# Performance work log

Hardware: AMD Instinct MI355X
Metric: run time of the kernel (lower is better)

The kernel has to match this reference:

```python
import jax, jax.numpy as jnp
import numpy as np

D_MODEL = 1024
N_HEADS = 16
D_FF = 4 * D_MODEL
CTX = 2048
EPS = 1e-5


def setup_inputs() -> dict:
    key = jax.random.key(0)
    ks = jax.random.split(key, 8)
    s = 0.02
    z = jax.random.normal(ks[0], (2, CTX, D_MODEL), dtype=jnp.float32)
    W_Q = jax.random.normal(ks[1], (D_MODEL, D_MODEL), dtype=jnp.float32) * s
    W_K = jax.random.normal(ks[2], (D_MODEL, D_MODEL), dtype=jnp.float32) * s
    W_V = jax.random.normal(ks[3], (D_MODEL, D_MODEL), dtype=jnp.float32) * s
    W_O = jax.random.normal(ks[4], (D_MODEL, D_MODEL), dtype=jnp.float32) * s
    W_fc = jax.random.normal(ks[5], (D_MODEL, D_FF), dtype=jnp.float32) * s
    W_proj = jax.random.normal(ks[6], (D_FF, D_MODEL), dtype=jnp.float32) * s
    g1 = jnp.ones((D_MODEL,), dtype=jnp.float32)
    g2 = jnp.ones((D_MODEL,), dtype=jnp.float32)
    return {"z": z, "W_Q": W_Q, "W_K": W_K, "W_V": W_V, "W_O": W_O,
            "W_fc": W_fc, "W_proj": W_proj, "g1": g1, "g2": g2}


def rmsnorm(x, gain):
    rms = jnp.sqrt(jnp.sum(x * x, axis=-1, keepdims=True) / x.shape[-1] + EPS)
    return (x / rms) * gain


def gelu_erf(x):
    return x * 0.5 * (1.0 + jax.lax.erf(x / jnp.sqrt(2.0).astype(x.dtype)))


def attention(zn, W_Q, W_K, W_V, W_O):
    B, T, D = zn.shape
    H = N_HEADS
    dh = D // H
    # [B,T,D] -> [B,H,T,dh]
    def split(x):
        return x.reshape(B, T, H, dh).transpose(0, 2, 1, 3)
    Q = split(zn @ W_Q)
    K = split(zn @ W_K)
    V = split(zn @ W_V)
    scores = jnp.einsum('bhtd,bhsd->bhts', Q, K) / jnp.sqrt(jnp.float32(dh))
    causal = jnp.triu(jnp.ones((T, T), dtype=bool), k=1)  # True above diagonal -> masked
    scores = jnp.where(causal[None, None], -jnp.inf, scores)
    weights = jax.nn.softmax(scores, axis=-1)
    ctx = jnp.einsum('bhts,bhsd->bhtd', weights, V)
    ctx = ctx.transpose(0, 2, 1, 3).reshape(B, T, D)
    return ctx @ W_O


def reference(z, W_Q, W_K, W_V, W_O, W_fc, W_proj, g1, g2):
    # pre-norm GPT block: z + attn(norm1(z)); then + ffn(norm2(z))
    z = z + attention(rmsnorm(z, g1), W_Q, W_K, W_V, W_O)
    h = rmsnorm(z, g2)
    ffn = gelu_erf(h @ W_fc) @ W_proj
    return z + ffn
```

## Files before the change

kernel.cpp:

```cpp
#include <hip/hip_runtime.h>
#include <hip/hip_bf16.h>
#include <math.h>


typedef __bf16 bf16x8 __attribute__((ext_vector_type(8)));
typedef float  f32x4  __attribute__((ext_vector_type(4)));

#define MFMA_16x16x32_BF16(A, B, C) __builtin_amdgcn_mfma_f32_16x16x32_bf16((A), (B), (C), 0, 0, 0)

#define GLDS16(g, l) __builtin_amdgcn_global_load_lds( \
    (const __attribute__((address_space(1))) void*)(g), \
    (__attribute__((address_space(3))) void*)(l), 16, 0, 0)

__global__ __launch_bounds__(256) void fused_head_kernel(
    const float* __restrict__ W_Q, const float* __restrict__ W_K,
    const float* __restrict__ W_V, const float* __restrict__ W_O,
    const float* __restrict__ W_fc, const float* __restrict__ W_proj,
    __bf16* __restrict__ WtQKV, __bf16* __restrict__ WtO,
    __bf16* __restrict__ Wtfc, __bf16* __restrict__ Wtproj,
    const float* __restrict__ z, const float* __restrict__ g1,
    __bf16* __restrict__ zn)
{
    const int id = blockIdx.x;
    if (id >= 12288) {
        const int row = id - 12288, t = threadIdx.x;
        const float4 v = ((const float4*)(z + (size_t)row * 1024))[t];
        float ss = v.x * v.x + v.y * v.y + v.z * v.z + v.w * v.w;
#pragma unroll
        for (int m = 1; m < 64; m <<= 1) ss += __shfl_xor(ss, m);
        __shared__ float red[4];
        const int wid = t >> 6, lane = t & 63;
        if (lane == 0) red[wid] = ss;
        __syncthreads();
        const float tot = red[0] + red[1] + red[2] + red[3];
        const float inv = rsqrtf(tot * (1.0f / 1024.0f) + 1e-5f);
        const float4 gv = ((const float4*)g1)[t];
        __bf16* o = zn + (size_t)row * 1024 + t * 4;
        o[0] = (__bf16)(v.x * inv * gv.x);
        o[1] = (__bf16)(v.y * inv * gv.y);
        o[2] = (__bf16)(v.z * inv * gv.z);
        o[3] = (__bf16)(v.w * inv * gv.w);
        return;
    }
    const float* src;
    __bf16* dst;
    int K, N, nx, t;
    if (id < 4096) {
        const int wsel = id >> 10;
        t = id & 1023;
        src = (wsel == 0) ? W_Q : (wsel == 1) ? W_K : (wsel == 2) ? W_V : W_O;
        dst = (wsel < 3) ? (WtQKV + (size_t)wsel * 1048576) : WtO;
        K = 1024; N = 1024; nx = 32;
    } else if (id < 8192) {
        t = id - 4096; src = W_fc; dst = Wtfc; K = 1024; N = 4096; nx = 128;
    } else {
        t = id - 8192; src = W_proj; dst = Wtproj; K = 4096; N = 1024; nx = 32;
    }
    const int n0 = (t % nx) * 32, k0 = (t / nx) * 32;

    __shared__ float tile[32][33];
    const int c = threadIdx.x & 31, r = threadIdx.x >> 5;
#pragma unroll
    for (int i = 0; i < 4; ++i)
        tile[r + 8 * i][c] = src[(size_t)(k0 + r + 8 * i) * N + n0 + c];
    __syncthreads();
#pragma unroll
    for (int i = 0; i < 4; ++i)
        dst[(size_t)(n0 + r + 8 * i) * K + k0 + c] = (__bf16)tile[c][r + 8 * i];
}

__global__ __launch_bounds__(256) void rmsnorm_kernel(
    const float* __restrict__ x, const float* __restrict__ gain,
    __bf16* __restrict__ out)
{
    const int row = blockIdx.x, t = threadIdx.x;
    const float4 v = ((const float4*)(x + (size_t)row * 1024))[t];
    float ss = v.x * v.x + v.y * v.y + v.z * v.z + v.w * v.w;
#pragma unroll
    for (int m = 1; m < 64; m <<= 1) ss += __shfl_xor(ss, m);
    __shared__ float red[4];
    const int wid = t >> 6, lane = t & 63;
    if (lane == 0) red[wid] = ss;
    __syncthreads();
    const float tot = red[0] + red[1] + red[2] + red[3];
    const float inv = rsqrtf(tot * (1.0f / 1024.0f) + 1e-5f);
    const float4 gv = ((const float4*)gain)[t];
    __bf16* o = out + (size_t)row * 1024 + t * 4;
    o[0] = (__bf16)(v.x * inv * gv.x);
    o[1] = (__bf16)(v.y * inv * gv.y);
    o[2] = (__bf16)(v.z * inv * gv.z);
    o[3] = (__bf16)(v.w * inv * gv.w);
}

__global__ __launch_bounds__(256) void reduce_add_kernel(
    float* __restrict__ out, const float* __restrict__ p0,
    const float* __restrict__ p1, int n4)
{
    for (int i = blockIdx.x * 256 + threadIdx.x; i < n4; i += gridDim.x * 256) {
        const float4 a = ((const float4*)p0)[i];
        const float4 b = ((const float4*)p1)[i];
        float4 o = ((float4*)out)[i];
        o.x += a.x + b.x; o.y += a.y + b.y;
        o.z += a.z + b.z; o.w += a.w + b.w;
        ((float4*)out)[i] = o;
    }
}

template <int EPI>
__device__ __forceinline__ void epi_write(
    void* outp, const float* res, int N, int rowg, int colg, float v)
{
    if constexpr (EPI == 1) {
        const size_t idx = (size_t)rowg * N + colg;
        ((float*)outp)[idx] = res[idx] + v;
    } else if constexpr (EPI == 2) {
        const size_t idx = (size_t)rowg * N + colg;
        const float u = v * (1.0f + 0.044715f * v * v) * 2.3022585093f;
        const float r = __builtin_amdgcn_rcpf(1.0f + exp2f(u));
        ((__bf16*)outp)[idx] = (__bf16)(v - v * r);
    } else if constexpr (EPI == 3) {
        const size_t idx = (size_t)rowg * N + colg;
        ((float*)outp)[idx] += v;
    } else {
        __bf16* base = (__bf16*)outp;
        const int seg = colg >> 10;
        const int cg = colg & 1023;
        if (seg < 2) {
            base[(size_t)seg * 4194304 + (size_t)rowg * 1024 + cg] = (__bf16)v;
        } else {
            const int tt = rowg & 2047;
            const int r32 = tt & 31;
            const int p = ((r32 & 12) << 1) | ((r32 >> 2) & 4) | (r32 & 3);
            base[8388608 +
                 ((size_t)((rowg >> 11) * 16 + (cg >> 6)) * 64 + (cg & 63)) * 2048 +
                 ((tt & ~31) | p)] = (__bf16)v;
        }
    }
}

template <int EPI>
__global__ __launch_bounds__(512, 2) void gemm256(
    const __bf16* __restrict__ A, const __bf16* __restrict__ Bt,
    void* __restrict__ outp, const float* __restrict__ res,
    int M, int N, int K)
{
    __shared__ __bf16 As[2][2][128 * 64];
    __shared__ __bf16 Bs[2][2][128 * 64];
    const int tid = threadIdx.x;

    const int gx = gridDim.x, nwg = gx * gridDim.y;
    int bid = blockIdx.y * gx + blockIdx.x;
    if ((nwg & 7) == 0) bid = (bid & 7) * (nwg >> 3) + (bid >> 3);
    const int m0 = (bid / gx) * 256, n0 = (bid % gx) * 256;

    const int lane = tid & 63, w = tid >> 6;
    const int wr = w >> 2, wc = w & 3;
    const int lr = lane & 15, g = lane >> 4;
    const int srow8 = lane >> 3, schunk = (lane & 7) ^ srow8;
    const int xk = lr & 7;
    const int wch = wc >> 1, bro = (wc & 1) * 64;

    const __bf16* Ab = A + (size_t)m0 * K;
    const __bf16* Bb = Bt + (size_t)n0 * K;

    auto STG = [&](const __bf16* gb, __bf16* lds, int kt, int half) {
        const __bf16* src = gb + (size_t)(half * 128) * K + (kt << 6);
#pragma unroll
        for (int j = 0; j < 2; ++j) {
            const int sidx = j * 8 + w;
            GLDS16(src + (size_t)(sidx * 8 + srow8) * K + schunk * 8, lds + sidx * 512);
        }
    };

    f32x4 acc[8][4] = {};
    bf16x8 af[2][4], bf[2][4];

#define LAF(BUF, QM) do {                                                       \
    _Pragma("unroll") for (int i_ = 0; i_ < 4; ++i_)                            \
    _Pragma("unroll") for (int kk_ = 0; kk_ < 2; ++kk_)                         \
        af[kk_][i_] = *(const bf16x8*)&As[BUF][wr]                              \
            [((QM) * 64 + i_ * 16 + lr) * 64 + (((kk_ * 4 + g) ^ xk) << 3)];    \
    } while (0)

#define LBF(BUF, QN) do {                                                       \
    _Pragma("unroll") for (int i_ = 0; i_ < 2; ++i_)                            \
    _Pragma("unroll") for (int kk_ = 0; kk_ < 2; ++kk_)                         \
        bf[kk_][(QN) * 2 + i_] = *(const bf16x8*)&Bs[BUF][wch]                  \
            [(bro + ((QN) * 2 + i_) * 16 + lr) * 64 + (((kk_ * 4 + g) ^ xk) << 3)]; \
    } while (0)

#define MMQ(QM, QN) do {                                                        \
    __builtin_amdgcn_s_setprio(1);                                              \
    _Pragma("unroll") for (int kk_ = 0; kk_ < 2; ++kk_)                         \
    _Pragma("unroll") for (int i_ = 0; i_ < 4; ++i_)                            \
    _Pragma("unroll") for (int n_ = 0; n_ < 2; ++n_)                            \
        acc[(QM) * 4 + i_][(QN) * 2 + n_] = MFMA_16x16x32_BF16(                 \
            af[kk_][i_], bf[kk_][(QN) * 2 + n_], acc[(QM) * 4 + i_][(QN) * 2 + n_]); \
    __builtin_amdgcn_s_setprio(0);                                              \
    } while (0)

#define BAR()  __builtin_amdgcn_s_barrier()
#define VMC(N_) asm volatile("s_waitcnt vmcnt(" #N_ ")" ::: "memory")
#define SGB0() __builtin_amdgcn_sched_barrier(0)

    const int nt = K >> 6, niter = nt >> 1;

    STG(Ab, &As[0][0][0], 0, 0); STG(Ab, &As[0][1][0], 0, 1);
    STG(Bb, &Bs[0][0][0], 0, 0); STG(Bb, &Bs[0][1][0], 0, 1);
    STG(Bb, &Bs[1][0][0], 1, 0); STG(Bb, &Bs[1][1][0], 1, 1);

    for (int i = 0; i < niter - 1; ++i) {
        const int t1 = 2 * i + 1;
        STG(Ab, &As[1][0][0], t1, 0);
        VMC(6); BAR(); SGB0();
        LAF(0, 0); LBF(0, 0); MMQ(0, 0); BAR();
        LBF(0, 1); STG(Ab, &As[1][1][0], t1, 1); BAR(); MMQ(0, 1); BAR();
        LAF(0, 1); STG(Bb, &Bs[0][0][0], t1 + 1, 0); BAR(); MMQ(1, 0); BAR();
        STG(Bb, &Bs[0][1][0], t1 + 1, 1); BAR(); MMQ(1, 1); BAR();
        STG(Ab, &As[0][0][0], t1 + 1, 0);
        VMC(6); BAR(); SGB0();
        LAF(1, 0); LBF(1, 0); MMQ(0, 0); BAR();
        LBF(1, 1); STG(Ab, &As[0][1][0], t1 + 1, 1); BAR(); MMQ(0, 1); BAR();
        LAF(1, 1); STG(Bb, &Bs[1][0][0], t1 + 2, 0); BAR(); MMQ(1, 0); BAR();
        STG(Bb, &Bs[1][1][0], t1 + 2, 1); BAR(); MMQ(1, 1); BAR();
    }
    {
        STG(Ab, &As[1][0][0], nt - 1, 0);
        VMC(6); BAR(); SGB0();
        LAF(0, 0); LBF(0, 0); MMQ(0, 0); BAR();
        LBF(0, 1); STG(Ab, &As[1][1][0], nt - 1, 1); BAR(); MMQ(0, 1); BAR();
        LAF(0, 1); BAR(); MMQ(1, 0); BAR();
        BAR(); MMQ(1, 1); BAR();
        VMC(0); BAR(); SGB0();
        LAF(1, 0); LBF(1, 0); MMQ(0, 0); BAR();
        LBF(1, 1); BAR(); MMQ(0, 1); BAR();
        LAF(1, 1); BAR(); MMQ(1, 0); BAR();
        BAR(); MMQ(1, 1); BAR();
    }
#undef LAF
#undef LBF
#undef MMQ
#undef BAR
#undef VMC
#undef SGB0

#pragma unroll
    for (int mi = 0; mi < 8; ++mi)
#pragma unroll
        for (int ni = 0; ni < 4; ++ni) {
            const int colg = n0 + wc * 64 + ni * 16 + lr;
#pragma unroll
            for (int r = 0; r < 4; ++r) {
                const int rowg = m0 + wr * 128 + mi * 16 + 4 * g + r;
                epi_write<EPI>(outp, res, N, rowg, colg, acc[mi][ni][r]);
            }
        }
}

template <int BM, int BN, int EPI>
__global__ __launch_bounds__(256) void gemm_bf16(
    const __bf16* __restrict__ A, const __bf16* __restrict__ Bt,
    void* __restrict__ outp, const float* __restrict__ res,
    int M, int N, int K, int Kld)
{
    __shared__ __bf16 As[2][BM * 64];
    __shared__ __bf16 Bs[2][BN * 64];
    const int tid = threadIdx.x;

    const int gx = gridDim.x, nwg = gx * gridDim.y;
    int bid = blockIdx.y * gx + blockIdx.x;
    if ((nwg & 7) == 0) bid = (bid & 7) * (nwg >> 3) + (bid >> 3);
    const int m0 = (bid / gx) * BM, n0 = (bid % gx) * BN;

    const int lane = tid & 63, w = tid >> 6;
    const int wm = w >> 1, wn = w & 1;
    const int lr = lane & 15, g = lane >> 4;
    const int srow = lane >> 3;
    const int scol = ((lane & 7) ^ srow) * 8;
    const int xr8 = lr & 7;

    constexpr int MI = BM / 32, NI = BN / 32;
    f32x4 acc[MI][NI] = {};

    const __bf16* Abase = A + (size_t)m0 * Kld + blockIdx.z * K;
    const __bf16* Bbase = Bt + (size_t)n0 * Kld + blockIdx.z * K;

    auto STAGE = [&](int kb, int buf) {
#pragma unroll
        for (int j = 0; j < BM / 32; ++j) {
            const int s = j * 4 + w;
            GLDS16(Abase + (size_t)(s * 8 + srow) * Kld + kb + scol, &As[buf][s * 512]);
        }
#pragma unroll
        for (int j = 0; j < BN / 32; ++j) {
            const int s = j * 4 + w;
            GLDS16(Bbase + (size_t)(s * 8 + srow) * Kld + kb + scol, &Bs[buf][s * 512]);
        }
    };

    const int nt = K >> 6;
    STAGE(0, 0);
    __syncthreads();

    for (int t = 0; t < nt; ++t) {
        const int cur = t & 1;
        if (t + 1 < nt) STAGE((t + 1) << 6, cur ^ 1);

        bf16x8 af[2][MI], bfr[2][NI];
#pragma unroll
        for (int kk = 0; kk < 2; ++kk) {
#pragma unroll
            for (int i = 0; i < MI; ++i)
                af[kk][i] = *(const bf16x8*)
                    &As[cur][(wm * (BM / 2) + i * 16 + lr) * 64 + (((kk * 4 + g) ^ xr8) << 3)];
#pragma unroll
            for (int i = 0; i < NI; ++i)
                bfr[kk][i] = *(const bf16x8*)
                    &Bs[cur][(wn * (BN / 2) + i * 16 + lr) * 64 + (((kk * 4 + g) ^ xr8) << 3)];
        }
#pragma unroll
        for (int kk = 0; kk < 2; ++kk)
#pragma unroll
            for (int mi = 0; mi < MI; ++mi)
#pragma unroll
                for (int ni = 0; ni < NI; ++ni)
                    acc[mi][ni] = MFMA_16x16x32_BF16(af[kk][mi], bfr[kk][ni], acc[mi][ni]);
        if (t + 1 < nt) __syncthreads();
    }

#pragma unroll
    for (int mi = 0; mi < MI; ++mi)
#pragma unroll
        for (int ni = 0; ni < NI; ++ni) {
            const int colg = n0 + wn * (BN / 2) + ni * 16 + lr;
#pragma unroll
            for (int r = 0; r < 4; ++r) {
                const int rowg = m0 + wm * (BM / 2) + mi * 16 + 4 * g + r;
                const float v = acc[mi][ni][r];
                if constexpr (EPI == 5) {
                    float* pout = (blockIdx.z == 0) ? (float*)outp : (float*)(void*)res;
                    pout[(size_t)rowg * N + colg] = v;
                } else {
                    epi_write<EPI>(outp, res, N, rowg, colg, v);
                }
            }
        }
}

__global__ __launch_bounds__(512) void attn_kernel(
    const __bf16* __restrict__ Q, const __bf16* __restrict__ Kb,
    const __bf16* __restrict__ Vt, __bf16* __restrict__ ctx)
{
    const int Dm = 1024, T = 2048;
    const int tid = threadIdx.x;
    const int w = tid >> 6, lane = tid & 63;
    const int lr = lane & 15, g = lane >> 4;
    const int bx = blockIdx.x;
    const int j = bx >> 5, bh = bx & 31, b = bh >> 4, h = bh & 15;
    const int qc = (j < 8) ? j : 23 - j;
    const int qbase = qc * 128 + w * 16;
    const size_t rowoff = (size_t)b * T;
    const __bf16* Qp = Q + rowoff * Dm + h * 64;
    const __bf16* Kp = Kb + rowoff * Dm + h * 64;
    const __bf16* Vtp = Vt + (size_t)bh * 64 * 2048;

    __shared__ __bf16 Ks[2][64 * 64];
    __shared__ __bf16 Vs[2][64 * 64];

    bf16x8 qf0 = *(const bf16x8*)&Qp[(size_t)(qbase + lr) * Dm + g * 8];
    bf16x8 qf1 = *(const bf16x8*)&Qp[(size_t)(qbase + lr) * Dm + 32 + g * 8];
    const float qsc = 0.125f * 1.44269504088896340736f;
#pragma unroll
    for (int jj = 0; jj < 8; ++jj) {
        qf0[jj] = (__bf16)((float)qf0[jj] * qsc);
        qf1[jj] = (__bf16)((float)qf1[jj] * qsc);
    }

    const int srow = lane >> 3;
    const int schunk = (lane & 7) ^ srow;
    const int wrow = w * 8 + srow;

    f32x4 acc[4] = {};
    float m_s = -__builtin_inff(), l_s = 0.0f;
    const int nsteps = 2 * qc + 2;
    const f32x4 zacc = {0.0f, 0.0f, 0.0f, 0.0f};
    const int xr = (lr & 7) << 3;
    const int qg = qbase + lr;

    GLDS16(Kp + (size_t)wrow * Dm + schunk * 8, &Ks[0][(w * 8) * 64]);
    GLDS16(Vtp + (size_t)wrow * T + schunk * 8, &Vs[0][(w * 8) * 64]);
    __syncthreads();

    for (int t = 0; t < nsteps; ++t) {
        const int kvb = t * 64, cur = t & 1;
        if (t + 1 < nsteps) {
            GLDS16(Kp + (size_t)(kvb + 64 + wrow) * Dm + schunk * 8,
                   &Ks[cur ^ 1][(w * 8) * 64]);
            GLDS16(Vtp + (size_t)wrow * T + kvb + 64 + schunk * 8,
                   &Vs[cur ^ 1][(w * 8) * 64]);
        }

        if (kvb <= qbase + 15) {
            float sv[4][4];
#pragma unroll
            for (int s4 = 0; s4 < 4; ++s4) {
                const int kv0 = kvb + s4 * 16;
                if (kv0 <= qbase + 15) {
                    const int row = s4 * 16 + lr;
                    const bf16x8 kfa = *(const bf16x8*)&Ks[cur][row * 64 + ((g * 8) ^ xr)];
                    const bf16x8 kfb = *(const bf16x8*)&Ks[cur][row * 64 + ((32 + g * 8) ^ xr)];
                    f32x4 st = MFMA_16x16x32_BF16(kfa, qf0, zacc);
                    st = MFMA_16x16x32_BF16(kfb, qf1, st);
                    const bool domask = (kv0 + 15 > qbase);
#pragma unroll
                    for (int r = 0; r < 4; ++r) {
                        float x = st[r];
                        if (domask && (kv0 + 4 * g + r > qg)) x = -__builtin_inff();
                        sv[s4][r] = x;
                    }
                } else {
#pragma unroll
                    for (int r = 0; r < 4; ++r) sv[s4][r] = -__builtin_inff();
                }
            }

            float tm = sv[0][0];
#pragma unroll
            for (int s4 = 0; s4 < 4; ++s4)
#pragma unroll
                for (int r = 0; r < 4; ++r) tm = fmaxf(tm, sv[s4][r]);
            tm = fmaxf(tm, __shfl_xor(tm, 16));
            tm = fmaxf(tm, __shfl_xor(tm, 32));

            float m_use = m_s;
            if (!__all(tm - m_s <= 11.5f)) {
                m_use = fmaxf(m_s, tm);
                const float corr = exp2f(m_s - m_use);
                l_s *= corr;
                float cr[4];
#pragma unroll
                for (int r = 0; r < 4; ++r) cr[r] = __shfl(corr, 4 * g + r);
#pragma unroll
                for (int ct = 0; ct < 4; ++ct) {
                    acc[ct][0] *= cr[0]; acc[ct][1] *= cr[1];
                    acc[ct][2] *= cr[2]; acc[ct][3] *= cr[3];
                }
                m_s = m_use;
            }

            float rs = 0.0f;
#pragma unroll
            for (int s4 = 0; s4 < 4; ++s4)
#pragma unroll
                for (int r = 0; r < 4; ++r) {
                    sv[s4][r] = exp2f(sv[s4][r] - m_use);
                    rs += sv[s4][r];
                }
            rs += __shfl_xor(rs, 16);
            rs += __shfl_xor(rs, 32);
            l_s += rs;

            bf16x8 pa0, pa1;
#pragma unroll
            for (int r = 0; r < 4; ++r) {
                pa0[r] = (__bf16)sv[0][r];
                pa0[4 + r] = (__bf16)sv[1][r];
                pa1[r] = (__bf16)sv[2][r];
                pa1[4 + r] = (__bf16)sv[3][r];
            }
            const bool liveB = (kvb + 32 <= qbase + 15);
#pragma unroll
            for (int ct = 0; ct < 4; ++ct) {
                const __bf16* vrow = &Vs[cur][(ct * 16 + lr) * 64];
                const bf16x8 vf = *(const bf16x8*)&vrow[(8 * g) ^ xr];
                acc[ct] = MFMA_16x16x32_BF16(pa0, vf, acc[ct]);
                if (liveB) {
                    const bf16x8 vf2 = *(const bf16x8*)&vrow[(32 + 8 * g) ^ xr];
                    acc[ct] = MFMA_16x16x32_BF16(pa1, vf2, acc[ct]);
                }
            }
        }
        __syncthreads();
    }

    const float il = __builtin_amdgcn_rcpf(l_s);
    float dn[4];
#pragma unroll
    for (int r = 0; r < 4; ++r) dn[r] = __shfl(il, 4 * g + r);
#pragma unroll
    for (int ct = 0; ct < 4; ++ct)
#pragma unroll
        for (int r = 0; r < 4; ++r)
            ctx[(rowoff + qbase + 4 * g + r) * Dm + h * 64 + ct * 16 + lr] =
                (__bf16)(acc[ct][r] * dn[r]);
}

extern "C" void kernel_launch(void* const* d_in, const int* in_sizes, int n_in,
                              void* d_out, int out_size, void* d_ws, size_t ws_size,
                              hipStream_t stream)
{
    (void)in_sizes; (void)n_in; (void)out_size; (void)ws_size;
    const float* z      = (const float*)d_in[0];
    const float* W_Q    = (const float*)d_in[1];
    const float* W_K    = (const float*)d_in[2];
    const float* W_V    = (const float*)d_in[3];
    const float* W_O    = (const float*)d_in[4];
    const float* W_fc   = (const float*)d_in[5];
    const float* W_proj = (const float*)d_in[6];
    const float* g1     = (const float*)d_in[7];
    const float* g2     = (const float*)d_in[8];
    float* out = (float*)d_out;

    char* ws = (char*)d_ws;
    const size_t MB = (size_t)1 << 20;
    __bf16* WtQKV  = (__bf16*)(ws + 0 * MB);
    __bf16* WtO    = (__bf16*)(ws + 6 * MB);
    __bf16* Wtfc   = (__bf16*)(ws + 8 * MB);
    __bf16* Wtproj = (__bf16*)(ws + 16 * MB);
    __bf16* zn     = (__bf16*)(ws + 24 * MB);
    __bf16* Qb     = (__bf16*)(ws + 32 * MB);
    __bf16* Kbuf   = (__bf16*)(ws + 40 * MB);
    __bf16* Vtb    = (__bf16*)(ws + 48 * MB);
    __bf16* ffn1   = (__bf16*)(ws + 40 * MB);
    float*  part0  = (float*)(ws + 0 * MB);
    float*  part1  = (float*)(ws + 24 * MB);
    __bf16* ctx    = zn;
    __bf16* hb     = Qb;

    const int Tt = 2048, Dm = 1024, Bb = 2, M = Bb * Tt, DFF = 4096;
    const dim3 blk256(256), blk512(512);

    fused_head_kernel<<<16384, blk256, 0, stream>>>(
        W_Q, W_K, W_V, W_O, W_fc, W_proj, WtQKV, WtO, Wtfc, Wtproj, z, g1, zn);

    gemm_bf16<128, 128, 4><<<dim3(24, 32), blk256, 0, stream>>>(
        zn, WtQKV, Qb, nullptr, M, 3072, Dm, Dm);

    attn_kernel<<<512, blk512, 0, stream>>>(Qb, Kbuf, Vtb, ctx);

    gemm_bf16<128, 64, 1><<<dim3(16, 32), blk256, 0, stream>>>(
        ctx, WtO, out, z, M, Dm, Dm, Dm);

    rmsnorm_kernel<<<M, blk256, 0, stream>>>(out, g2, hb);

    gemm256<2><<<dim3(16, 16), blk512, 0, stream>>>(
        hb, Wtfc, ffn1, nullptr, M, DFF, Dm);

    gemm_bf16<128, 128, 5><<<dim3(8, 32, 2), blk256, 0, stream>>>(
        ffn1, Wtproj, part0, (const float*)part1, M, Dm, DFF / 2, DFF);

    reduce_add_kernel<<<2048, blk256, 0, stream>>>(out, part0, part1, M * Dm / 4);
}
```

Measured before the change: 250.4 us.

## Double the attention KV tile from 64 to 128 keys per step

The flash-attention loop now processes 128 keys per iteration instead of 64. This halves the number of barrier-synchronised steps and prefetch issues, with K/V staging split into two loads per thread and a new XOR swizzle for the wider V tile. In exchange it doubles shared memory per block, increases register pressure (sv now holds 8x4 scores), and wastes more masked work on the diagonal tiles.

```diff
diff --git a/kernel.cpp b/kernel.cpp
--- a/kernel.cpp
+++ b/kernel.cpp
@@ -364,8 +364,8 @@
     const __bf16* Kp = Kb + rowoff * Dm + h * 64;
     const __bf16* Vtp = Vt + (size_t)bh * 64 * 2048;
 
-    __shared__ __bf16 Ks[2][64 * 64];
-    __shared__ __bf16 Vs[2][64 * 64];
+    __shared__ __bf16 Ks[2][128 * 64];
+    __shared__ __bf16 Vs[2][64 * 128];
 
     bf16x8 qf0 = *(const bf16x8*)&Qp[(size_t)(qbase + lr) * Dm + g * 8];
     bf16x8 qf1 = *(const bf16x8*)&Qp[(size_t)(qbase + lr) * Dm + 32 + g * 8];
@@ -376,107 +376,113 @@
         qf1[jj] = (__bf16)((float)qf1[jj] * qsc);
     }
 
-    const int srow = lane >> 3;
-    const int schunk = (lane & 7) ^ srow;
-    const int wrow = w * 8 + srow;
+    const int ksrow = lane >> 3;
+    const int kschunk = (lane & 7) ^ ksrow;
+    const int vsrow = lane >> 4;
 
     f32x4 acc[4] = {};
     float m_s = -__builtin_inff(), l_s = 0.0f;
-    const int nsteps = 2 * qc + 2;
+    const int nsteps = qc + 1;
     const f32x4 zacc = {0.0f, 0.0f, 0.0f, 0.0f};
-    const int xr = (lr & 7) << 3;
+    const int x8 = lr & 7;
     const int qg = qbase + lr;
 
-    GLDS16(Kp + (size_t)wrow * Dm + schunk * 8, &Ks[0][(w * 8) * 64]);
-    GLDS16(Vtp + (size_t)wrow * T + schunk * 8, &Vs[0][(w * 8) * 64]);
+    auto STAGE = [&](int kvb, int buf) {
+#pragma unroll
+        for (int jj = 0; jj < 2; ++jj) {
+            const int krow = w * 16 + jj * 8;
+            GLDS16(Kp + (size_t)(kvb + krow + ksrow) * Dm + kschunk * 8,
+                   &Ks[buf][krow * 64]);
+            const int vrow = w * 8 + jj * 4;
+            const int vchunk = (lane & 15) ^ ((vrow + vsrow) & 15);
+            GLDS16(Vtp + (size_t)(vrow + vsrow) * T + kvb + vchunk * 8,
+                   &Vs[buf][vrow * 128]);
+        }
+    };
+
+    STAGE(0, 0);
     __syncthreads();
 
     for (int t = 0; t < nsteps; ++t) {
-        const int kvb = t * 64, cur = t & 1;
-        if (t + 1 < nsteps) {
-            GLDS16(Kp + (size_t)(kvb + 64 + wrow) * Dm + schunk * 8,
-                   &Ks[cur ^ 1][(w * 8) * 64]);
-            GLDS16(Vtp + (size_t)wrow * T + kvb + 64 + schunk * 8,
-                   &Vs[cur ^ 1][(w * 8) * 64]);
-        }
-
-        if (kvb <= qbase + 15) {
-            float sv[4][4];
-#pragma unroll
-            for (int s4 = 0; s4 < 4; ++s4) {
-                const int kv0 = kvb + s4 * 16;
-                if (kv0 <= qbase + 15) {
-                    const int row = s4 * 16 + lr;
-                    const bf16x8 kfa = *(const bf16x8*)&Ks[cur][row * 64 + ((g * 8) ^ xr)];
-                    const bf16x8 kfb = *(const bf16x8*)&Ks[cur][row * 64 + ((32 + g * 8) ^ xr)];
-                    f32x4 st = MFMA_16x16x32_BF16(kfa, qf0, zacc);
-                    st = MFMA_16x16x32_BF16(kfb, qf1, st);
-                    const bool domask = (kv0 + 15 > qbase);
-#pragma unroll
-                    for (int r = 0; r < 4; ++r) {
-                        float x = st[r];
-                        if (domask && (kv0 + 4 * g + r > qg)) x = -__builtin_inff();
-                        sv[s4][r] = x;
-                    }
-                } else {
-#pragma unroll
-                    for (int r = 0; r < 4; ++r) sv[s4][r] = -__builtin_inff();
+        const int kvb = t * 128, cur = t & 1;
+        if (t + 1 < nsteps) STAGE(kvb + 128, cur ^ 1);
+
+        float sv[8][4];
+#pragma unroll
+        for (int s4 = 0; s4 < 8; ++s4) {
+            const int kv0 = kvb + s4 * 16;
+            if (kv0 <= qbase + 15) {
+                const int row = s4 * 16 + lr;
+                const bf16x8 kfa = *(const bf16x8*)&Ks[cur][row * 64 + ((g ^ x8) << 3)];
+                const bf16x8 kfb = *(const bf16x8*)&Ks[cur][row * 64 + (((4 + g) ^ x8) << 3)];
+                f32x4 st = MFMA_16x16x32_BF16(kfa, qf0, zacc);
+                st = MFMA_16x16x32_BF16(kfb, qf1, st);
+                const bool domask = (kv0 + 15 > qbase);
+#pragma unroll
+                for (int r = 0; r < 4; ++r) {
+                    float x = st[r];
+                    if (domask && (kv0 + 4 * g + r > qg)) x = -__builtin_inff();
+                    sv[s4][r] = x;
                 }
-            }
-
-            float tm = sv[0][0];
-#pragma unroll
-            for (int s4 = 0; s4 < 4; ++s4)
-#pragma unroll
-                for (int r = 0; r < 4; ++r) tm = fmaxf(tm, sv[s4][r]);
-            tm = fmaxf(tm, __shfl_xor(tm, 16));
-            tm = fmaxf(tm, __shfl_xor(tm, 32));
-
-            float m_use = m_s;
-            if (!__all(tm - m_s <= 11.5f)) {
-                m_use = fmaxf(m_s, tm);
-                const float corr = exp2f(m_s - m_use);
-                l_s *= corr;
-                float cr[4];
-#pragma unroll
-                for (int r = 0; r < 4; ++r) cr[r] = __shfl(corr, 4 * g + r);
-#pragma unroll
-                for (int ct = 0; ct < 4; ++ct) {
-                    acc[ct][0] *= cr[0]; acc[ct][1] *= cr[1];
-                    acc[ct][2] *= cr[2]; acc[ct][3] *= cr[3];
-                }
-                m_s = m_use;
-            }
-
-            float rs = 0.0f;
-#pragma unroll
-            for (int s4 = 0; s4 < 4; ++s4)
-#pragma unroll
-                for (int r = 0; r < 4; ++r) {
-                    sv[s4][r] = exp2f(sv[s4][r] - m_use);
-                    rs += sv[s4][r];
-                }
-            rs += __shfl_xor(rs, 16);
-            rs += __shfl_xor(rs, 32);
-            l_s += rs;
-
-            bf16x8 pa0, pa1;
+            } else {
+#pragma unroll
+                for (int r = 0; r < 4; ++r) sv[s4][r] = -__builtin_inff();
+            }
+        }
+
+        float tm = sv[0][0];
+#pragma unroll
+        for (int s4 = 0; s4 < 8; ++s4)
+#pragma unroll
+            for (int r = 0; r < 4; ++r) tm = fmaxf(tm, sv[s4][r]);
+        tm = fmaxf(tm, __shfl_xor(tm, 16));
+        tm = fmaxf(tm, __shfl_xor(tm, 32));
+
+        float m_use = m_s;
+        if (!__all(tm - m_s <= 11.5f)) {
+            m_use = fmaxf(m_s, tm);
+            const float corr = exp2f(m_s - m_use);
+            l_s *= corr;
+            float cr[4];
+#pragma unroll
+            for (int r = 0; r < 4; ++r) cr[r] = __shfl(corr, 4 * g + r);
+#pragma unroll
+            for (int ct = 0; ct < 4; ++ct) {
+                acc[ct][0] *= cr[0]; acc[ct][1] *= cr[1];
+                acc[ct][2] *= cr[2]; acc[ct][3] *= cr[3];
+            }
+            m_s = m_use;
+        }
+
+        float rs = 0.0f;
+#pragma unroll
+        for (int s4 = 0; s4 < 8; ++s4)
 #pragma unroll
             for (int r = 0; r < 4; ++r) {
-                pa0[r] = (__bf16)sv[0][r];
-                pa0[4 + r] = (__bf16)sv[1][r];
-                pa1[r] = (__bf16)sv[2][r];
-                pa1[4 + r] = (__bf16)sv[3][r];
-            }
-            const bool liveB = (kvb + 32 <= qbase + 15);
-#pragma unroll
-            for (int ct = 0; ct < 4; ++ct) {
-                const __bf16* vrow = &Vs[cur][(ct * 16 + lr) * 64];
-                const bf16x8 vf = *(const bf16x8*)&vrow[(8 * g) ^ xr];
-                acc[ct] = MFMA_16x16x32_BF16(pa0, vf, acc[ct]);
-                if (liveB) {
-                    const bf16x8 vf2 = *(const bf16x8*)&vrow[(32 + 8 * g) ^ xr];
-                    acc[ct] = MFMA_16x16x32_BF16(pa1, vf2, acc[ct]);
+                sv[s4][r] = exp2f(sv[s4][r] - m_use);
+                rs += sv[s4][r];
+            }
+        rs += __shfl_xor(rs, 16);
+        rs += __shfl_xor(rs, 32);
+        l_s += rs;
+
+        bf16x8 pa[4];
+#pragma unroll
+        for (int s = 0; s < 4; ++s)
+#pragma unroll
+            for (int r = 0; r < 4; ++r) {
+                pa[s][r] = (__bf16)sv[2 * s][r];
+                pa[s][4 + r] = (__bf16)sv[2 * s + 1][r];
+            }
+#pragma unroll
+        for (int ct = 0; ct < 4; ++ct) {
+            const __bf16* vrow = &Vs[cur][(ct * 16 + lr) * 128];
+#pragma unroll
+            for (int s = 0; s < 4; ++s) {
+                if (kvb + s * 32 <= qbase + 15) {
+                    const bf16x8 vf =
+                        *(const bf16x8*)&vrow[(((s * 4 + g) ^ lr) << 3)];
+                    acc[ct] = MFMA_16x16x32_BF16(pa[s], vf, acc[ct]);
                 }
             }
         }
```

Measured after the change: 246.4 us. No clear change (-1.6%).
